# Performance work log

Measured on AMD Instinct MI355X. Metric: run time of the kernel, lower is better.

## Reference

```python
import jax, jax.numpy as jnp
import numpy as np

IN_C = 64
OUT_C = 128
HEADS = 8
DIM = 9 * IN_C  # 576


def unfold3x3_s2(fea):
    # torch.nn.functional.unfold(fea, (3,3), padding=1, stride=2)
    # returns [N, C*9, L] with channel-major (c, kh, kw) ordering.
    N, C, H, W = fea.shape
    Ho, Wo = H // 2, W // 2
    p = jnp.pad(fea, ((0, 0), (0, 0), (1, 1), (1, 1)))
    patches = jnp.stack(
        [p[:, :, ki:ki + 2 * Ho:2, kj:kj + 2 * Wo:2] for ki in range(3) for kj in range(3)],
        axis=2,
    )  # [N, C, 9, Ho, Wo]
    return patches.reshape(N, C * 9, Ho * Wo)


def mhsa(x, w_qkv, b_qkv, w_out, b_out):
    # standard ViT attention: x [B, L, D]
    B, L, D = x.shape
    dh = D // HEADS
    qkv = x @ w_qkv + b_qkv  # [B, L, 3D]
    q, k, v = jnp.split(qkv, 3, axis=-1)
    def heads(t):
        return t.reshape(B, L, HEADS, dh).transpose(0, 2, 1, 3)  # [B, h, L, dh]
    q, k, v = heads(q), heads(k), heads(v)
    scale = dh ** -0.5
    scores = jnp.einsum('bhqd,bhkd->bhqk', q, k) * scale
    attn = jax.nn.softmax(scores, axis=-1)
    o = jnp.einsum('bhqk,bhkd->bhqd', attn, v)  # [B, h, L, dh]
    o = o.transpose(0, 2, 1, 3).reshape(B, L, D)
    return o @ w_out + b_out


def setup_inputs() -> dict:
    key = jax.random.key(0)
    ks = jax.random.split(key, 6)
    s = DIM ** -0.5
    return {
        'fea': jax.random.normal(ks[0], (1, IN_C, 128, 128), dtype=jnp.float32),
        'w_qkv': jax.random.normal(ks[1], (DIM, 3 * DIM), dtype=jnp.float32) * s,
        'b_qkv': jnp.zeros((3 * DIM,), dtype=jnp.float32),
        'w_out': jax.random.normal(ks[2], (DIM, DIM), dtype=jnp.float32) * s,
        'b_out': jnp.zeros((DIM,), dtype=jnp.float32),
        'conv_w': jax.random.normal(ks[3], (OUT_C, IN_C, 3, 3), dtype=jnp.float32) * s,
    }


def reference(fea, w_qkv, b_qkv, w_out, b_out, conv_w):
    N, C, H, W = fea.shape
    Ho, Wo = H // 2, W // 2
    x = unfold3x3_s2(fea).transpose(0, 2, 1)          # [N, L, 9C]
    x = mhsa(x, w_qkv, b_qkv, w_out, b_out) + x       # residual
    # matmul with reshaped conv weights: [N, L, 9C] @ [9C, out_c]
    y = x @ conv_w.reshape(OUT_C, -1).T               # [N, L, out_c]
    y = y.transpose(0, 2, 1).reshape(N, OUT_C, Ho, Wo)  # fold with (1,1) kernel
    return jax.nn.silu(y)
```

## Files before the change

kernel.cpp:

```cpp
#include <hip/hip_runtime.h>
#include <hip/hip_bf16.h>
#include <math.h>

#define L_TOK 4096
#define D_DIM 576
#define NHEADS 8
#define DHEAD 72
#define DPAD 96
#define HSZ ((size_t)NHEADS * L_TOK * DPAD)
#define KSPLIT 4
#define LOG2E 1.4426950408889634f
#define SCALE2 (0.11785113019775792f * 1.4426950408889634f)

typedef __attribute__((ext_vector_type(8))) short short8;
typedef __attribute__((ext_vector_type(4))) short short4v;
typedef __attribute__((ext_vector_type(4))) float float4v;

union F4S8 {
  float4 f4;
  short8 s8;
  __hip_bfloat16 h[8];
};

__device__ inline void tc_body(const float* __restrict__ src,
                               __hip_bfloat16* __restrict__ dst, int R, int C,
                               int bi, int bj, int t, __hip_bfloat16* Ts) {
  const int col = t & 63, row4 = t >> 6;
#pragma unroll
  for (int u = 0; u < 16; u++) {
    int r = u * 4 + row4;
    Ts[r * 68 + col] = __float2bfloat16(src[(size_t)(bj * 64 + r) * C + bi * 64 + col]);
  }
  __syncthreads();
#pragma unroll
  for (int u = 0; u < 16; u++) {
    int c = u * 4 + row4;
    dst[(size_t)(bi * 64 + c) * R + bj * 64 + col] = Ts[col * 68 + c];
  }
}

__global__ __launch_bounds__(256) void prep_all(const float* __restrict__ fea,
                                                const float* __restrict__ w_qkv,
                                                const float* __restrict__ w_out,
                                                const float* __restrict__ conv_w,
                                                __hip_bfloat16* __restrict__ xb,
                                                __hip_bfloat16* __restrict__ WqkvT,
                                                __hip_bfloat16* __restrict__ WoT,
                                                __hip_bfloat16* __restrict__ CwB) {
  __shared__ float Shm[3120];
  const int b = blockIdx.x;
  const int t = threadIdx.x;
  if (b < 512) {
    float* Lf = Shm;
    const int ho = b & 63;
    const int c0 = (b >> 6) * 8;
    for (int e = t; e < 3072; e += 256) {
      int c = e / 384;
      int rr = (e / 128) % 3;
      int w = e & 127;
      int h = 2 * ho + rr - 1;
      float v = 0.f;
      if ((unsigned)h < 128u) v = fea[(size_t)(c0 + c) * 16384 + h * 128 + w];
      Lf[(c * 3 + rr) * 130 + w + 1] = v;
    }
    if (t < 24) { Lf[t * 130] = 0.f; Lf[t * 130 + 129] = 0.f; }
    __syncthreads();
    for (int e = t; e < 576; e += 256) {
      int wo = e / 9, ch = e - wo * 9;
      F4S8 u;
#pragma unroll
      for (int j = 0; j < 8; j++) {
        int dd = ch * 8 + j;
        int c = dd / 9, k = dd - c * 9;
        int ki = k / 3, kj = k - ki * 3;
        u.h[j] = __float2bfloat16(Lf[(c * 3 + ki) * 130 + 2 * wo + kj]);
      }
      *(float4*)(xb + (size_t)(ho * 64 + wo) * D_DIM + c0 * 9 + ch * 8) = u.f4;
    }
  } else if (b < 755) {
    int bb = b - 512;
    tc_body(w_qkv, WqkvT, D_DIM, 1728, bb % 27, bb / 27, t, (__hip_bfloat16*)Shm);
  } else if (b < 836) {
    int bb = b - 755;
    tc_body(w_out, WoT, D_DIM, D_DIM, bb % 9, bb / 9, t, (__hip_bfloat16*)Shm);
  } else {
    int i = (b - 836) * 256 + t;
    CwB[i] = __float2bfloat16(conv_w[i]);
  }
}

template <int EPI, int NMI>
__global__ __launch_bounds__(256) void gemm_mfma(const __hip_bfloat16* __restrict__ A,
                                                 const __hip_bfloat16* __restrict__ Bt,
                                                 const float* __restrict__ bias,
                                                 const __hip_bfloat16* __restrict__ resid,
                                                 __hip_bfloat16* __restrict__ outB,
                                                 __hip_bfloat16* __restrict__ outB2) {
  constexpr int K = D_DIM;
  constexpr int BM = NMI * 32;
  __shared__ __align__(16) __hip_bfloat16 As[BM * 72];
  __shared__ __align__(16) __hip_bfloat16 Bs[64 * 72];
  const int t = threadIdx.x;
  const int wave = t >> 6, lane = t & 63, quad = lane >> 4, l16 = lane & 15;
  const int wm = (wave & 2) * (NMI * 8);
  const int wn = (wave & 1) * 32;
  const int m0 = blockIdx.x * BM, n0 = blockIdx.y * 64;

  float4v acc[NMI][2];
#pragma unroll
  for (int i = 0; i < NMI; i++)
#pragma unroll
    for (int j = 0; j < 2; j++) acc[i][j] = (float4v){0.f, 0.f, 0.f, 0.f};

  const int arow = t >> 3, ach = t & 7;
  for (int k0 = 0; k0 < K; k0 += 64) {
    __syncthreads();
#pragma unroll
    for (int u = 0; u < NMI; u++) {
      int row = u * 32 + arow;
      *(float4*)(&As[row * 72 + ach * 8]) =
          *(const float4*)(A + (size_t)(m0 + row) * K + k0 + ach * 8);
    }
#pragma unroll
    for (int u = 0; u < 2; u++) {
      int row = u * 32 + arow;
      *(float4*)(&Bs[row * 72 + ach * 8]) =
          *(const float4*)(Bt + (size_t)(n0 + row) * K + k0 + ach * 8);
    }
    __syncthreads();
    short8 af[NMI][2], bfr[2][2];
#pragma unroll
    for (int i = 0; i < NMI; i++)
#pragma unroll
      for (int s = 0; s < 2; s++)
        af[i][s] = *(const short8*)(&As[(wm + i * 16 + l16) * 72 + s * 32 + quad * 8]);
#pragma unroll
    for (int j = 0; j < 2; j++)
#pragma unroll
      for (int s = 0; s < 2; s++)
        bfr[j][s] = *(const short8*)(&Bs[(wn + j * 16 + l16) * 72 + s * 32 + quad * 8]);
#pragma unroll
    for (int i = 0; i < NMI; i++)
#pragma unroll
      for (int j = 0; j < 2; j++) {
        acc[i][j] = __builtin_amdgcn_mfma_f32_16x16x32_bf16(af[i][0], bfr[j][0], acc[i][j], 0, 0, 0);
        acc[i][j] = __builtin_amdgcn_mfma_f32_16x16x32_bf16(af[i][1], bfr[j][1], acc[i][j], 0, 0, 0);
      }
  }

  if (EPI == 0) {
    const int part = n0 / D_DIM;
    if (part < 2) {
      __hip_bfloat16* dst = outB + (size_t)part * HSZ;
      const float sc = (part == 0) ? SCALE2 : 1.f;
#pragma unroll
      for (int j = 0; j < 2; j++) {
        int ng = n0 + wn + j * 16 + l16;
        float bv = bias[ng];
        int rem = ng - part * D_DIM;
        int h = rem / DHEAD;
        int d = rem - h * DHEAD;
#pragma unroll
        for (int i = 0; i < NMI; i++) {
          int mb = m0 + wm + i * 16 + quad * 4;
#pragma unroll
          for (int r = 0; r < 4; r++)
            dst[((size_t)h * L_TOK + mb + r) * DPAD + d] =
                __float2bfloat16((acc[i][j][r] + bv) * sc);
        }
      }
    } else {
      __hip_bfloat16* Ls = As;
      __syncthreads();
      const int n0rel = n0 - 2 * D_DIM;
#pragma unroll
      for (int j = 0; j < 2; j++) {
        int nloc = wn + j * 16 + l16;
        float bv = bias[n0 + nloc];
#pragma unroll
        for (int i = 0; i < NMI; i++) {
          int mloc = wm + i * 16 + quad * 4;
#pragma unroll
          for (int r = 0; r < 4; r++)
            Ls[nloc * 136 + mloc + r] = __float2bfloat16(acc[i][j][r] + bv);
        }
      }
      __syncthreads();
      for (int e = t; e < 1024; e += 256) {
        int row = e >> 4, ch = e & 15;
        int ng = n0rel + row;
        int hh = ng / DHEAD, dd = ng - hh * DHEAD;
        *(float4*)(outB2 + ((size_t)hh * DPAD + dd) * L_TOK + m0 + ch * 8) =
            *(const float4*)(&Ls[row * 136 + ch * 8]);
      }
    }
  } else {
#pragma unroll
    for (int j = 0; j < 2; j++) {
      int ng = n0 + wn + j * 16 + l16;
      float bv = bias[ng];
#pragma unroll
      for (int i = 0; i < NMI; i++) {
        int mb = m0 + wm + i * 16 + quad * 4;
#pragma unroll
        for (int r = 0; r < 4; r++) {
          size_t idx = (size_t)(mb + r) * D_DIM + ng;
          float v = acc[i][j][r] + bv + __bfloat162float(resid[idx]);
          outB[idx] = __float2bfloat16(v);
        }
      }
    }
  }
}

__global__ __launch_bounds__(256) void final_small(const __hip_bfloat16* __restrict__ A,
                                                   const __hip_bfloat16* __restrict__ Bt,
                                                   float* __restrict__ out) {
  __shared__ __align__(16) __hip_bfloat16 As[32 * 72];
  __shared__ __align__(16) __hip_bfloat16 Bs[32 * 72];
  const int t = threadIdx.x;
  const int wave = t >> 6, lane = t & 63, quad = lane >> 4, l16 = lane & 15;
  const int wm = (wave & 2) * 8;
  const int wn = (wave & 1) * 16;
  const int m0 = blockIdx.x * 32, n0 = blockIdx.y * 32;

  float4v acc = (float4v){0.f, 0.f, 0.f, 0.f};

  const int arow = t >> 3, ach = t & 7;
  for (int k0 = 0; k0 < D_DIM; k0 += 64) {
    __syncthreads();
    *(float4*)(&As[arow * 72 + ach * 8]) =
        *(const float4*)(A + (size_t)(m0 + arow) * D_DIM + k0 + ach * 8);
    *(float4*)(&Bs[arow * 72 + ach * 8]) =
        *(const float4*)(Bt + (size_t)(n0 + arow) * D_DIM + k0 + ach * 8);
    __syncthreads();
    short8 af[2], bfr[2];
#pragma unroll
    for (int s = 0; s < 2; s++) {
      af[s] = *(const short8*)(&As[(wm + l16) * 72 + s * 32 + quad * 8]);
      bfr[s] = *(const short8*)(&Bs[(wn + l16) * 72 + s * 32 + quad * 8]);
    }
    acc = __builtin_amdgcn_mfma_f32_16x16x32_bf16(af[0], bfr[0], acc, 0, 0, 0);
    acc = __builtin_amdgcn_mfma_f32_16x16x32_bf16(af[1], bfr[1], acc, 0, 0, 0);
  }
  const int oc = n0 + wn + l16;
  const int mb = m0 + wm + quad * 4;
#pragma unroll
  for (int r = 0; r < 4; r++) {
    float v = acc[r];
    float sg = 1.f / (1.f + __expf(-v));
    out[(size_t)oc * L_TOK + mb + r] = v * sg;
  }
}

#define KS_STRIDE 104
#define VT_STRIDE 72
#define PS_STRIDE 40
#define KBUF (64 * KS_STRIDE)
#define VBUF (80 * VT_STRIDE)

__global__ __launch_bounds__(256, 2) void attn_mfma(const __hip_bfloat16* __restrict__ Qb,
                                                    const __hip_bfloat16* __restrict__ Kb,
                                                    const __hip_bfloat16* __restrict__ VbT,
                                                    __hip_bfloat16* __restrict__ Opart,
                                                    float* __restrict__ Ml) {
  __shared__ __align__(16) __hip_bfloat16 Ks[2 * KBUF];
  __shared__ __align__(16) __hip_bfloat16 Vt[2 * VBUF];
  __shared__ __align__(16) __hip_bfloat16 Ps[4 * 64 * PS_STRIDE];

  const int bid = blockIdx.x;
  const int h = bid & 7;
  const int rest = bid >> 3;
  const int ksp = rest & 3;
  const int qblk = rest >> 2;
  const int t = threadIdx.x;
  const int wave = t >> 6;
  const int lane = t & 63;
  const int quad = lane >> 4;
  const int l16 = lane & 15;

  const __hip_bfloat16* Qh = Qb + (size_t)h * L_TOK * DPAD;
  const __hip_bfloat16* Kh = Kb + (size_t)h * L_TOK * DPAD;
  const __hip_bfloat16* VhT = VbT + (size_t)h * DPAD * L_TOK;

  const int qbase = qblk * 256 + wave * 64;
  short8 qf[4][3];
#pragma unroll
  for (int mi = 0; mi < 4; mi++) {
#pragma unroll
    for (int s = 0; s < 3; s++) {
      if (s == 2 && quad >= 1) {
        qf[mi][s] = (short8){0, 0, 0, 0, 0, 0, 0, 0};
        if (quad == 1) qf[mi][s][0] = (short)0xC100;
      } else {
        qf[mi][s] = *(const short8*)(Qh + (size_t)(qbase + mi * 16 + l16) * DPAD + s * 32 + quad * 8);
      }
    }
  }

  const float4 zero4 = {0.f, 0.f, 0.f, 0.f};
  union { float4 f4; unsigned u[4]; } kpad, vones;
  kpad.u[0] = 0x00003F80u; kpad.u[1] = 0u; kpad.u[2] = 0u; kpad.u[3] = 0u;
  vones.u[0] = vones.u[1] = vones.u[2] = vones.u[3] = 0x3F803F80u;
  if (t < 192) {
    int row = t / 3, ch = 9 + t % 3;
    float4 kv = (ch == 9) ? kpad.f4 : zero4;
    *(float4*)(&Ks[row * KS_STRIDE + ch * 8]) = kv;
    *(float4*)(&Ks[KBUF + row * KS_STRIDE + ch * 8]) = kv;
  } else {
    int e = t - 192;
    int d = 72 + (e >> 3), ch = e & 7;
    float4 vv = (d == 72) ? vones.f4 : zero4;
    *(float4*)(&Vt[d * VT_STRIDE + ch * 8]) = vv;
    *(float4*)(&Vt[VBUF + d * VT_STRIDE + ch * 8]) = vv;
  }

  float4v Of[4][5];
#pragma unroll
  for (int mi = 0; mi < 4; mi++)
#pragma unroll
    for (int nt = 0; nt < 5; nt++) Of[mi][nt] = (float4v){0.f, 0.f, 0.f, 0.f};

  __hip_bfloat16* myPs = Ps + wave * 64 * PS_STRIDE;
  const int kstart = ksp * 1024;

  int kgo[3], klo[3], vgo[3], vlo[3];
#pragma unroll
  for (int u = 0; u < 3; u++) {
    int e = t + u * 256;
    int ee = (e < 576) ? e : 0;
    int row = ee / 9, ch = ee - row * 9;
    kgo[u] = row * (DPAD * 2) + ch * 16;
    klo[u] = row * (KS_STRIDE * 2) + ch * 16;
    int d = ee >> 3, c2 = ee & 7;
    vgo[u] = d * (L_TOK * 2) + c2 * 16;
    vlo[u] = d * (VT_STRIDE * 2) + c2 * 16;
  }
  const bool has3 = (t < 64);

  float4 krg0, krg1, krg2, vrg0, vrg1, vrg2;
  auto stage_load = [&](int kbase) {
    const char* Kt_ = (const char*)(Kh + (size_t)kbase * DPAD);
    const char* Vg_ = (const char*)(VhT + kbase);
    krg0 = *(const float4*)(Kt_ + kgo[0]);
    krg1 = *(const float4*)(Kt_ + kgo[1]);
    vrg0 = *(const float4*)(Vg_ + vgo[0]);
    vrg1 = *(const float4*)(Vg_ + vgo[1]);
    if (has3) {
      krg2 = *(const float4*)(Kt_ + kgo[2]);
      vrg2 = *(const float4*)(Vg_ + vgo[2]);
    }
  };
  auto stage_write = [&](__hip_bfloat16* Kw, __hip_bfloat16* Vw) {
    *(float4*)((char*)Kw + klo[0]) = krg0;
    *(float4*)((char*)Kw + klo[1]) = krg1;
    *(float4*)((char*)Vw + vlo[0]) = vrg0;
    *(float4*)((char*)Vw + vlo[1]) = vrg1;
    if (has3) {
      *(float4*)((char*)Kw + klo[2]) = krg2;
      *(float4*)((char*)Vw + vlo[2]) = vrg2;
    }
  };

  auto body = [&](int kt, const __hip_bfloat16* Ksb, const __hip_bfloat16* Vtb,
                  __hip_bfloat16* Kw, __hip_bfloat16* Vw) {
    const int knext = (kt < 15) ? kt + 1 : 15;
    stage_load(kstart + knext * 64);

    float4v S[4][4];
    __builtin_amdgcn_s_setprio(1);
#pragma unroll
    for (int ks = 0; ks < 4; ks++) {
      float4v a0 = (float4v){0.f, 0.f, 0.f, 0.f};
      float4v a1 = a0, a2 = a0, a3 = a0;
#pragma unroll
      for (int s = 0; s < 3; s++) {
        short8 kf = *(const short8*)(&Ksb[(ks * 16 + l16) * KS_STRIDE + s * 32 + quad * 8]);
        a0 = __builtin_amdgcn_mfma_f32_16x16x32_bf16(kf, qf[0][s], a0, 0, 0, 0);
        a1 = __builtin_amdgcn_mfma_f32_16x16x32_bf16(kf, qf[1][s], a1, 0, 0, 0);
        a2 = __builtin_amdgcn_mfma_f32_16x16x32_bf16(kf, qf[2][s], a2, 0, 0, 0);
        a3 = __builtin_amdgcn_mfma_f32_16x16x32_bf16(kf, qf[3][s], a3, 0, 0, 0);
      }
#pragma unroll
      for (int r = 0; r < 4; r++) {
        S[0][ks][r] = a0[r]; S[1][ks][r] = a1[r];
        S[2][ks][r] = a2[r]; S[3][ks][r] = a3[r];
      }
    }
    __builtin_amdgcn_s_setprio(0);

#pragma unroll
    for (int kstep = 0; kstep < 2; kstep++) {
#pragma unroll
      for (int mi = 0; mi < 4; mi++) {
#pragma unroll
        for (int k2 = 0; k2 < 2; k2++) {
          int ks = kstep * 2 + k2;
          union { short4v v; __hip_bfloat16 hh[4]; } pk;
#pragma unroll
          for (int r = 0; r < 4; r++)
            pk.hh[r] = __float2bfloat16(exp2f(S[mi][ks][r]));
          *(short4v*)(&myPs[(mi * 16 + l16) * PS_STRIDE + k2 * 16 + quad * 4]) = pk.v;
        }
      }
      short8 pa[4];
#pragma unroll
      for (int mi = 0; mi < 4; mi++)
        pa[mi] = *(const short8*)(&myPs[(mi * 16 + l16) * PS_STRIDE + quad * 8]);
      __builtin_amdgcn_s_setprio(1);
#pragma unroll
      for (int nt = 0; nt < 5; nt++) {
        short8 vb = *(const short8*)(&Vtb[(nt * 16 + l16) * VT_STRIDE + kstep * 32 + quad * 8]);
        Of[0][nt] = __builtin_amdgcn_mfma_f32_16x16x32_bf16(pa[0], vb, Of[0][nt], 0, 0, 0);
        Of[1][nt] = __builtin_amdgcn_mfma_f32_16x16x32_bf16(pa[1], vb, Of[1][nt], 0, 0, 0);
        Of[2][nt] = __builtin_amdgcn_mfma_f32_16x16x32_bf16(pa[2], vb, Of[2][nt], 0, 0, 0);
        Of[3][nt] = __builtin_amdgcn_mfma_f32_16x16x32_bf16(pa[3], vb, Of[3][nt], 0, 0, 0);
      }
      __builtin_amdgcn_s_setprio(0);
    }

    stage_write(Kw, Vw);
    __syncthreads();
  };

  stage_load(kstart);
  stage_write(Ks, Vt);
  __syncthreads();

  for (int kt2 = 0; kt2 < 16; kt2 += 2) {
    body(kt2,     Ks,        Vt,        Ks + KBUF, Vt + VBUF);
    body(kt2 + 1, Ks + KBUF, Vt + VBUF, Ks,        Vt);
  }

  const size_t pb = ((size_t)ksp * NHEADS + h) * L_TOK;
#pragma unroll
  for (int mi = 0; mi < 4; mi++) {
#pragma unroll
    for (int nt = 0; nt < 5; nt++) {
      int d = nt * 16 + l16;
      if (d < DHEAD) {
#pragma unroll
        for (int r = 0; r < 4; r++) {
          int q = qbase + mi * 16 + quad * 4 + r;
          Opart[(pb + q) * 72 + d] = __float2bfloat16(Of[mi][nt][r]);
        }
      }
    }
  }
  if (l16 == 8) {
#pragma unroll
    for (int mi = 0; mi < 4; mi++) {
#pragma unroll
      for (int r = 0; r < 4; r++)
        Ml[pb + qbase + mi * 16 + quad * 4 + r] = Of[mi][4][r];
    }
  }
}

__global__ __launch_bounds__(256) void attn_merge(const __hip_bfloat16* __restrict__ Opart,
                                                  const float* __restrict__ Ml,
                                                  __hip_bfloat16* __restrict__ ob) {
  int idx = blockIdx.x * 256 + threadIdx.x;
  int h = idx / (L_TOK * 9);
  int rem = idx - h * (L_TOK * 9);
  int q = rem / 9;
  int ch = rem - q * 9;
  float denom = 0.f;
  float acc[8] = {0, 0, 0, 0, 0, 0, 0, 0};
#pragma unroll
  for (int s = 0; s < KSPLIT; s++) {
    size_t b = ((size_t)s * NHEADS + h) * L_TOK + q;
    denom += Ml[b];
    short8 o = *(const short8*)(Opart + b * 72 + ch * 8);
#pragma unroll
    for (int j = 0; j < 8; j++) {
      union { short ss; __hip_bfloat16 bb; } u;
      u.ss = o[j];
      acc[j] += __bfloat162float(u.bb);
    }
  }
  float inv = 1.f / denom;
  __hip_bfloat16* dst = ob + (size_t)q * D_DIM + h * DHEAD + ch * 8;
#pragma unroll
  for (int j = 0; j < 8; j++) dst[j] = __float2bfloat16(acc[j] * inv);
}

extern "C" void kernel_launch(void* const* d_in, const int* in_sizes, int n_in,
                              void* d_out, int out_size, void* d_ws, size_t ws_size,
                              hipStream_t stream) {
  const float* fea    = (const float*)d_in[0];
  const float* w_qkv  = (const float*)d_in[1];
  const float* b_qkv  = (const float*)d_in[2];
  const float* w_out  = (const float*)d_in[3];
  const float* b_out  = (const float*)d_in[4];
  const float* conv_w = (const float*)d_in[5];
  float* out = (float*)d_out;

  __hip_bfloat16* xb    = (__hip_bfloat16*)d_ws;
  __hip_bfloat16* WqkvT = xb + (size_t)L_TOK * D_DIM;
  __hip_bfloat16* WoT   = WqkvT + (size_t)1728 * D_DIM;
  __hip_bfloat16* CwB   = WoT + (size_t)D_DIM * D_DIM;
  __hip_bfloat16* QKb   = CwB + (size_t)128 * D_DIM;
  __hip_bfloat16* VbT   = QKb + 2 * HSZ;
  __hip_bfloat16* Opart = VbT + HSZ;
  float* Ml = (float*)(Opart + (size_t)KSPLIT * NHEADS * L_TOK * 72);
  __hip_bfloat16* ob = QKb;
  __hip_bfloat16* xr = Opart;

  prep_all<<<1124, 256, 0, stream>>>(fea, w_qkv, w_out, conv_w, xb, WqkvT, WoT, CwB);
  gemm_mfma<0, 4><<<dim3(32, 27), 256, 0, stream>>>(xb, WqkvT, b_qkv, nullptr, QKb, VbT);
  attn_mfma<<<512, 256, 0, stream>>>(QKb, QKb + HSZ, VbT, Opart, Ml);
  attn_merge<<<1152, 256, 0, stream>>>(Opart, Ml, ob);
  gemm_mfma<1, 2><<<dim3(64, 9), 256, 0, stream>>>(ob, WoT, b_out, xb, xr, nullptr);
  final_small<<<dim3(128, 4), 256, 0, stream>>>(xr, CwB, out);
}
```

Measured before the change: 178.6 us.

## Halve attention query tile per wave and drop LDS double buffering for occupancy

Measured after the change: 191.9 us. 7.5% more time.

```diff
diff --git a/kernel.cpp b/kernel.cpp
--- a/kernel.cpp
+++ b/kernel.cpp
@@ -259,14 +259,14 @@
 #define KBUF (64 * KS_STRIDE)
 #define VBUF (80 * VT_STRIDE)
 
-__global__ __launch_bounds__(256, 2) void attn_mfma(const __hip_bfloat16* __restrict__ Qb,
+__global__ __launch_bounds__(256, 4) void attn_mfma(const __hip_bfloat16* __restrict__ Qb,
                                                     const __hip_bfloat16* __restrict__ Kb,
                                                     const __hip_bfloat16* __restrict__ VbT,
                                                     __hip_bfloat16* __restrict__ Opart,
                                                     float* __restrict__ Ml) {
-  __shared__ __align__(16) __hip_bfloat16 Ks[2 * KBUF];
-  __shared__ __align__(16) __hip_bfloat16 Vt[2 * VBUF];
-  __shared__ __align__(16) __hip_bfloat16 Ps[4 * 64 * PS_STRIDE];
+  __shared__ __align__(16) __hip_bfloat16 Ks[KBUF];
+  __shared__ __align__(16) __hip_bfloat16 Vt[VBUF];
+  __shared__ __align__(16) __hip_bfloat16 Ps[4 * 32 * PS_STRIDE];
 
   const int bid = blockIdx.x;
   const int h = bid & 7;
@@ -283,10 +283,10 @@
   const __hip_bfloat16* Kh = Kb + (size_t)h * L_TOK * DPAD;
   const __hip_bfloat16* VhT = VbT + (size_t)h * DPAD * L_TOK;
 
-  const int qbase = qblk * 256 + wave * 64;
-  short8 qf[4][3];
-#pragma unroll
-  for (int mi = 0; mi < 4; mi++) {
+  const int qbase = qblk * 128 + wave * 32;
+  short8 qf[2][3];
+#pragma unroll
+  for (int mi = 0; mi < 2; mi++) {
 #pragma unroll
     for (int s = 0; s < 3; s++) {
       if (s == 2 && quad >= 1) {
@@ -304,24 +304,20 @@
   vones.u[0] = vones.u[1] = vones.u[2] = vones.u[3] = 0x3F803F80u;
   if (t < 192) {
     int row = t / 3, ch = 9 + t % 3;
-    float4 kv = (ch == 9) ? kpad.f4 : zero4;
-    *(float4*)(&Ks[row * KS_STRIDE + ch * 8]) = kv;
-    *(float4*)(&Ks[KBUF + row * KS_STRIDE + ch * 8]) = kv;
+    *(float4*)(&Ks[row * KS_STRIDE + ch * 8]) = (ch == 9) ? kpad.f4 : zero4;
   } else {
     int e = t - 192;
     int d = 72 + (e >> 3), ch = e & 7;
-    float4 vv = (d == 72) ? vones.f4 : zero4;
-    *(float4*)(&Vt[d * VT_STRIDE + ch * 8]) = vv;
-    *(float4*)(&Vt[VBUF + d * VT_STRIDE + ch * 8]) = vv;
-  }
-
-  float4v Of[4][5];
-#pragma unroll
-  for (int mi = 0; mi < 4; mi++)
+    *(float4*)(&Vt[d * VT_STRIDE + ch * 8]) = (d == 72) ? vones.f4 : zero4;
+  }
+
+  float4v Of[2][5];
+#pragma unroll
+  for (int mi = 0; mi < 2; mi++)
 #pragma unroll
     for (int nt = 0; nt < 5; nt++) Of[mi][nt] = (float4v){0.f, 0.f, 0.f, 0.f};
 
-  __hip_bfloat16* myPs = Ps + wave * 64 * PS_STRIDE;
+  __hip_bfloat16* myPs = Ps + wave * 32 * PS_STRIDE;
   const int kstart = ksp * 1024;
 
   int kgo[3], klo[3], vgo[3], vlo[3];
@@ -339,60 +335,53 @@
   const bool has3 = (t < 64);
 
   float4 krg0, krg1, krg2, vrg0, vrg1, vrg2;
-  auto stage_load = [&](int kbase) {
+  auto load_K = [&](int kbase) {
     const char* Kt_ = (const char*)(Kh + (size_t)kbase * DPAD);
-    const char* Vg_ = (const char*)(VhT + kbase);
     krg0 = *(const float4*)(Kt_ + kgo[0]);
     krg1 = *(const float4*)(Kt_ + kgo[1]);
+    if (has3) krg2 = *(const float4*)(Kt_ + kgo[2]);
+  };
+  auto load_V = [&](int kbase) {
+    const char* Vg_ = (const char*)(VhT + kbase);
     vrg0 = *(const float4*)(Vg_ + vgo[0]);
     vrg1 = *(const float4*)(Vg_ + vgo[1]);
+    if (has3) vrg2 = *(const float4*)(Vg_ + vgo[2]);
+  };
+  auto stage_write = [&]() {
+    *(float4*)((char*)Ks + klo[0]) = krg0;
+    *(float4*)((char*)Ks + klo[1]) = krg1;
+    *(float4*)((char*)Vt + vlo[0]) = vrg0;
+    *(float4*)((char*)Vt + vlo[1]) = vrg1;
     if (has3) {
-      krg2 = *(const float4*)(Kt_ + kgo[2]);
-      vrg2 = *(const float4*)(Vg_ + vgo[2]);
+      *(float4*)((char*)Ks + klo[2]) = krg2;
+      *(float4*)((char*)Vt + vlo[2]) = vrg2;
     }
   };
-  auto stage_write = [&](__hip_bfloat16* Kw, __hip_bfloat16* Vw) {
-    *(float4*)((char*)Kw + klo[0]) = krg0;
-    *(float4*)((char*)Kw + klo[1]) = krg1;
-    *(float4*)((char*)Vw + vlo[0]) = vrg0;
-    *(float4*)((char*)Vw + vlo[1]) = vrg1;
-    if (has3) {
-      *(float4*)((char*)Kw + klo[2]) = krg2;
-      *(float4*)((char*)Vw + vlo[2]) = vrg2;
-    }
-  };
-
-  auto body = [&](int kt, const __hip_bfloat16* Ksb, const __hip_bfloat16* Vtb,
-                  __hip_bfloat16* Kw, __hip_bfloat16* Vw) {
-    const int knext = (kt < 15) ? kt + 1 : 15;
-    stage_load(kstart + knext * 64);
-
-    float4v S[4][4];
+
+  auto compute = [&](int knext_base, bool prefetch) {
+    float4v S[2][4];
     __builtin_amdgcn_s_setprio(1);
 #pragma unroll
     for (int ks = 0; ks < 4; ks++) {
       float4v a0 = (float4v){0.f, 0.f, 0.f, 0.f};
-      float4v a1 = a0, a2 = a0, a3 = a0;
+      float4v a1 = a0;
 #pragma unroll
       for (int s = 0; s < 3; s++) {
-        short8 kf = *(const short8*)(&Ksb[(ks * 16 + l16) * KS_STRIDE + s * 32 + quad * 8]);
+        short8 kf = *(const short8*)(&Ks[(ks * 16 + l16) * KS_STRIDE + s * 32 + quad * 8]);
         a0 = __builtin_amdgcn_mfma_f32_16x16x32_bf16(kf, qf[0][s], a0, 0, 0, 0);
         a1 = __builtin_amdgcn_mfma_f32_16x16x32_bf16(kf, qf[1][s], a1, 0, 0, 0);
-        a2 = __builtin_amdgcn_mfma_f32_16x16x32_bf16(kf, qf[2][s], a2, 0, 0, 0);
-        a3 = __builtin_amdgcn_mfma_f32_16x16x32_bf16(kf, qf[3][s], a3, 0, 0, 0);
-      }
-#pragma unroll
-      for (int r = 0; r < 4; r++) {
-        S[0][ks][r] = a0[r]; S[1][ks][r] = a1[r];
-        S[2][ks][r] = a2[r]; S[3][ks][r] = a3[r];
-      }
+      }
+#pragma unroll
+      for (int r = 0; r < 4; r++) { S[0][ks][r] = a0[r]; S[1][ks][r] = a1[r]; }
     }
     __builtin_amdgcn_s_setprio(0);
 
+    if (prefetch) load_V(knext_base);
+
 #pragma unroll
     for (int kstep = 0; kstep < 2; kstep++) {
 #pragma unroll
-      for (int mi = 0; mi < 4; mi++) {
+      for (int mi = 0; mi < 2; mi++) {
 #pragma unroll
         for (int k2 = 0; k2 < 2; k2++) {
           int ks = kstep * 2 + k2;
@@ -403,38 +392,39 @@
           *(short4v*)(&myPs[(mi * 16 + l16) * PS_STRIDE + k2 * 16 + quad * 4]) = pk.v;
         }
       }
-      short8 pa[4];
-#pragma unroll
-      for (int mi = 0; mi < 4; mi++)
+      short8 pa[2];
+#pragma unroll
+      for (int mi = 0; mi < 2; mi++)
         pa[mi] = *(const short8*)(&myPs[(mi * 16 + l16) * PS_STRIDE + quad * 8]);
       __builtin_amdgcn_s_setprio(1);
 #pragma unroll
       for (int nt = 0; nt < 5; nt++) {
-        short8 vb = *(const short8*)(&Vtb[(nt * 16 + l16) * VT_STRIDE + kstep * 32 + quad * 8]);
+        short8 vb = *(const short8*)(&Vt[(nt * 16 + l16) * VT_STRIDE + kstep * 32 + quad * 8]);
         Of[0][nt] = __builtin_amdgcn_mfma_f32_16x16x32_bf16(pa[0], vb, Of[0][nt], 0, 0, 0);
         Of[1][nt] = __builtin_amdgcn_mfma_f32_16x16x32_bf16(pa[1], vb, Of[1][nt], 0, 0, 0);
-        Of[2][nt] = __builtin_amdgcn_mfma_f32_16x16x32_bf16(pa[2], vb, Of[2][nt], 0, 0, 0);
-        Of[3][nt] = __builtin_amdgcn_mfma_f32_16x16x32_bf16(pa[3], vb, Of[3][nt], 0, 0, 0);
       }
       __builtin_amdgcn_s_setprio(0);
     }
-
-    stage_write(Kw, Vw);
-    __syncthreads();
   };
 
-  stage_load(kstart);
-  stage_write(Ks, Vt);
+  load_K(kstart);
+  load_V(kstart);
+  stage_write();
   __syncthreads();
 
-  for (int kt2 = 0; kt2 < 16; kt2 += 2) {
-    body(kt2,     Ks,        Vt,        Ks + KBUF, Vt + VBUF);
-    body(kt2 + 1, Ks + KBUF, Vt + VBUF, Ks,        Vt);
-  }
+  for (int kt = 0; kt < 15; kt++) {
+    const int knext = kstart + (kt + 1) * 64;
+    load_K(knext);
+    compute(knext, true);
+    __syncthreads();
+    stage_write();
+    __syncthreads();
+  }
+  compute(kstart, false);
 
   const size_t pb = ((size_t)ksp * NHEADS + h) * L_TOK;
 #pragma unroll
-  for (int mi = 0; mi < 4; mi++) {
+  for (int mi = 0; mi < 2; mi++) {
 #pragma unroll
     for (int nt = 0; nt < 5; nt++) {
       int d = nt * 16 + l16;
@@ -449,7 +439,7 @@
   }
   if (l16 == 8) {
 #pragma unroll
-    for (int mi = 0; mi < 4; mi++) {
+    for (int mi = 0; mi < 2; mi++) {
 #pragma unroll
       for (int r = 0; r < 4; r++)
         Ml[pb + qbase + mi * 16 + quad * 4 + r] = Of[mi][4][r];
@@ -509,7 +499,7 @@
 
   prep_all<<<1124, 256, 0, stream>>>(fea, w_qkv, w_out, conv_w, xb, WqkvT, WoT, CwB);
   gemm_mfma<0, 4><<<dim3(32, 27), 256, 0, stream>>>(xb, WqkvT, b_qkv, nullptr, QKb, VbT);
-  attn_mfma<<<512, 256, 0, stream>>>(QKb, QKb + HSZ, VbT, Opart, Ml);
+  attn_mfma<<<1024, 256, 0, stream>>>(QKb, QKb + HSZ, VbT, Opart, Ml);
   attn_merge<<<1152, 256, 0, stream>>>(Opart, Ml, ob);
   gemm_mfma<1, 2><<<dim3(64, 9), 256, 0, stream>>>(ob, WoT, b_out, xb, xr, nullptr);
   final_small<<<dim3(128, 4), 256, 0, stream>>>(xr, CwB, out);
```
